# Performance work log

Measured on AMD Instinct MI355X. Metric: run time of the kernel, lower is better.

The kernel has to match this reference:

```python
import jax, jax.numpy as jnp
import numpy as np

ALPHA = 1.0
MIN_FEATURE_SIZE = 1.0
SC = 1e-12                      # stabilizer added to first derivatives
EPS_V_FLOOR = 1e-32 / 6.0       # torch.tensor(1e-32 ** 1 / 6) == 1e-32/6 (** binds tighter than /)


def _grad2d(phi, d):
    """Vectorized equivalent of numerical_gradient_2d: central differences in the
    interior, one-sided forward/backward differences at the boundaries."""
    gx = jnp.concatenate([
        (phi[1:2, :] - phi[0:1, :]) / d,           # forward diff at i == 0
        (phi[2:, :] - phi[:-2, :]) / (2.0 * d),    # central diff in interior
        (phi[-1:, :] - phi[-2:-1, :]) / d,         # backward diff at i == H-1
    ], axis=0)
    gy = jnp.concatenate([
        (phi[:, 1:2] - phi[:, 0:1]) / d,
        (phi[:, 2:] - phi[:, :-2]) / (2.0 * d),
        (phi[:, -1:] - phi[:, -2:-1]) / d,
    ], axis=1)
    return gx, gy


def setup_inputs() -> dict:
    key = jax.random.key(0)
    eps = jax.random.normal(key, (4096, 4096), dtype=jnp.float32)
    grid_size = jnp.asarray(0.05, dtype=jnp.float32)
    return {"eps": eps, "grid_size": grid_size}


def reference(eps, grid_size):
    # mirror the field along axis 1 (torch.cat((eps, eps.flip(1)), dim=1)) -> [H, 2W]
    eps = jnp.concatenate([eps, eps[:, ::-1]], axis=1)

    # ls_derivatives: first derivatives (+SC), then second derivatives of those
    eps_x, eps_y = _grad2d(eps, grid_size)
    eps_x = eps_x + SC
    eps_y = eps_y + SC
    eps_xx, eps_xy = _grad2d(eps_x, grid_size)
    _, eps_yy = _grad2d(eps_y, grid_size)

    pi_d = np.pi / (1.1 * MIN_FEATURE_SIZE)
    eps_v = jnp.maximum(jnp.sqrt(eps_x**2 + eps_y**2), EPS_V_FLOOR)
    k = (eps_x**2 * eps_yy - 2.0 * eps_x * eps_y * eps_xy + eps_y**2 * eps_xx) / eps_v**3
    curve_const = jnp.abs(k * jnp.arctan(eps_v / eps)) - pi_d
    return jnp.nansum(ALPHA * jnp.maximum(curve_const, 0.0) * grid_size**2)
```

## Files before the change

### kernel.cpp

```cpp
#include <hip/hip_runtime.h>
#include <math.h>


#define BLOCK_X 256
#define ROWS_PER 16

typedef float f32x2 __attribute__((ext_vector_type(2)));

__device__ __forceinline__ f32x2 mk2(float a, float b) { f32x2 v; v.x = a; v.y = b; return v; }
__device__ __forceinline__ f32x2 sp2(float a) { return mk2(a, a); }

#if __has_builtin(__builtin_elementwise_fma)
__device__ __forceinline__ f32x2 fma2(f32x2 a, f32x2 b, f32x2 c) { return __builtin_elementwise_fma(a, b, c); }
#else
__device__ __forceinline__ f32x2 fma2(f32x2 a, f32x2 b, f32x2 c) { return mk2(fmaf(a.x, b.x, c.x), fmaf(a.y, b.y, c.y)); }
#endif
#if __has_builtin(__builtin_elementwise_max)
__device__ __forceinline__ f32x2 max2(f32x2 a, f32x2 b) { return __builtin_elementwise_max(a, b); }
#else
__device__ __forceinline__ f32x2 max2(f32x2 a, f32x2 b) { return mk2(fmaxf(a.x, b.x), fmaxf(a.y, b.y)); }
#endif
__device__ __forceinline__ f32x2 abs2(f32x2 a) { return mk2(fabsf(a.x), fabsf(a.y)); }


__device__ __forceinline__ float fast_atan_ratio(float v, float c, float rv)
{
    const float rc = __builtin_amdgcn_rcpf(c);
    const float q  = v * rc;
    const float iq = c * rv;
    const bool  big = fabsf(q) > 1.0f;
    const float t  = big ? iq : q;
    const float s  = t * t;
    float p = fmaf(s, -0.01172120f, 0.05265332f);
    p = fmaf(s, p, -0.11643287f);
    p = fmaf(s, p,  0.19354346f);
    p = fmaf(s, p, -0.33262347f);
    p = fmaf(s, p,  0.99997726f);
    const float at = p * t;
    const float hp = copysignf(1.57079632679f, q);
    return big ? (hp - at) : at;
}

__device__ __forceinline__ f32x2 fast_atan_ratio2(f32x2 v, f32x2 c, f32x2 rvv)
{
    const f32x2 rc = mk2(__builtin_amdgcn_rcpf(c.x), __builtin_amdgcn_rcpf(c.y));
    const f32x2 q  = v * rc;
    const f32x2 iq = c * rvv;
    const bool big0 = fabsf(q.x) > 1.0f, big1 = fabsf(q.y) > 1.0f;
    const f32x2 t = mk2(big0 ? iq.x : q.x, big1 ? iq.y : q.y);
    const f32x2 s = t * t;
    f32x2 p = fma2(s, sp2(-0.01172120f), sp2(0.05265332f));
    p = fma2(s, p, sp2(-0.11643287f));
    p = fma2(s, p, sp2( 0.19354346f));
    p = fma2(s, p, sp2(-0.33262347f));
    p = fma2(s, p, sp2( 0.99997726f));
    const f32x2 at = p * t;
    const float hp0 = copysignf(1.57079632679f, q.x);
    const float hp1 = copysignf(1.57079632679f, q.y);
    return mk2(big0 ? (hp0 - at.x) : at.x, big1 ? (hp1 - at.y) : at.y);
}

template<bool XE>
__device__ __forceinline__ void load6(const float* __restrict__ rowp, int j0,
                                      bool left, bool right,
                                      f32x2& m, f32x2& c, f32x2& p)
{
    c = *reinterpret_cast<const f32x2*>(rowp + j0);
    if (XE) {
        const float* ma = rowp + (left  ? j0 : j0 - 2);
        const float* pa = rowp + (right ? j0 : j0 + 2);
        m = *reinterpret_cast<const f32x2*>(ma);
        p = *reinterpret_cast<const f32x2*>(pa);
        if (left)  m = mk2(c.x, c.x);
        if (right) p = mk2(c.y, c.x);
    } else {
        m = *reinterpret_cast<const f32x2*>(rowp + j0 - 2);
        p = *reinterpret_cast<const f32x2*>(rowp + j0 + 2);
    }
}

template<bool XE>
__device__ __forceinline__ f32x2 strip_packed(
    const float* __restrict__ eps, int Wn, int i0, int j0,
    bool left, bool right, float rd2, f32x2 syjv, f32x2 symv)
{
    const f32x2 SC2    = sp2(1e-12f);
    const float FLOORV = (float)(1e-32 / 6.0);
    const float pi_d   = 3.14159265358979323846f / 1.1f;

    const float* r0 = eps + (size_t)(i0 - 2) * (size_t)Wn;
    f32x2 A = *reinterpret_cast<const f32x2*>(r0 + j0);
    f32x2 Bm, Bc, Bp, Cm, Cc, Cp, Dm, Dc, Dp, Em, Ec, Ep;
    load6<XE>(r0 + (size_t)Wn,     j0, left, right, Bm, Bc, Bp);
    load6<XE>(r0 + (size_t)2 * Wn, j0, left, right, Cm, Cc, Cp);
    load6<XE>(r0 + (size_t)3 * Wn, j0, left, right, Dm, Dc, Dp);
    load6<XE>(r0 + (size_t)4 * Wn, j0, left, right, Em, Ec, Ep);
    const float* pr = r0 + (size_t)5 * Wn;

    f32x2 acc = sp2(0.0f);
    #pragma unroll 4
    for (int r = 0; r < ROWS_PER; ++r) {
        f32x2 Fm, Fc, Fp;
        load6<XE>(pr, j0, left, right, Fm, Fc, Fp);
        pr += Wn;

        const f32x2 ex  = fma2(Dc - Bc, sp2(rd2), SC2);
        const f32x2 Cl1 = mk2(Cm.y, Cc.x), Cr1 = mk2(Cc.y, Cp.x);
        const f32x2 ey  = fma2(Cr1 - Cl1, syjv, SC2);
        const f32x2 exn = fma2(Cc - A,  sp2(rd2), SC2);
        const f32x2 exs = fma2(Ec - Cc, sp2(rd2), SC2);
        const f32x2 exx = (exs - exn) * rd2;
        f32x2 eyw = fma2(Cc - Cm, symv, SC2);
        const f32x2 eye = fma2(Cp - Cc, sp2(rd2), SC2);
        if (XE) { if (left) eyw.x = ey.x; }
        const f32x2 eyy = (eye - eyw) * syjv;
        const f32x2 Bl1 = mk2(Bm.y, Bc.x), Br1 = mk2(Bc.y, Bp.x);
        const f32x2 Dl1 = mk2(Dm.y, Dc.x), Dr1 = mk2(Dc.y, Dp.x);
        const f32x2 exy = ((Dr1 - Br1) - (Dl1 - Bl1)) * (syjv * rd2);

        const f32x2 t1 = ex * ex, t2 = ey * ey;
        f32x2 num = t1 * eyy;
        num = fma2(t2, exx, num);
        num = fma2((ex * ey) * -2.0f, exy, num);
        const f32x2 ssum = t1 + t2;
        float ev0 = __builtin_amdgcn_sqrtf(ssum.x);
        float ev1 = __builtin_amdgcn_sqrtf(ssum.y);
        ev0 = fmaxf(ev0, FLOORV);
        ev1 = fmaxf(ev1, FLOORV);
        const f32x2 evv = mk2(ev0, ev1);
        const f32x2 rvv = mk2(__builtin_amdgcn_rcpf(ev0), __builtin_amdgcn_rcpf(ev1));
        const f32x2 k   = num * (rvv * rvv) * rvv;
        const f32x2 at  = fast_atan_ratio2(evv, Cc, rvv);
        const f32x2 cc  = abs2(k * at) - sp2(pi_d);
        acc = acc + max2(cc, sp2(0.0f));

        A  = Bc;
        Bm = Cm; Bc = Cc; Bp = Cp;
        Cm = Dm; Cc = Dc; Cp = Dp;
        Dm = Em; Dc = Ec; Dp = Ep;
        Em = Fm; Ec = Fc; Ep = Fp;
    }
    return acc;
}

__device__ float strip_scalar_yb(const float* __restrict__ eps, int Hn, int Wn,
                                 int i0, int j, float rd, float rd2)
{
    const float SC     = 1e-12f;
    const float FLOORV = (float)(1e-32 / 6.0);
    const float pi_d   = 3.14159265358979323846f / 1.1f;

    const int jm  = (j > 0) ? j - 1 : 0;
    const int jmm = (j > 1) ? j - 2 : 0;
    const int jp = j + 1, jpp = j + 2;
    const int cjp  = (jp  < Wn) ? jp  : (2 * Wn - 1 - jp);
    const int cjpp = (jpp < Wn) ? jpp : (2 * Wn - 1 - jpp);
    const bool jz = (j == 0);
    const float syj = jz ? rd : rd2;
    const float sym = (jm == 0) ? rd : rd2;

    auto rp = [&](int t) -> const float* {
        int tt = t < 0 ? 0 : t;
        tt = tt > Hn - 1 ? Hn - 1 : tt;
        return eps + (size_t)tt * (size_t)Wn;
    };

    float a2 = rp(i0 - 2)[j],   a1 = rp(i0 - 1)[j],  a0 = rp(i0)[j];
    float b1 = rp(i0 + 1)[j],   b2 = rp(i0 + 2)[j];
    float wN = rp(i0 - 1)[jm],  w0 = rp(i0)[jm],     wS = rp(i0 + 1)[jm];
    float eN = rp(i0 - 1)[cjp], e0 = rp(i0)[cjp],    eS = rp(i0 + 1)[cjp];
    float ww = rp(i0)[jmm],     ee = rp(i0)[cjpp];

    float acc = 0.0f;
    #pragma unroll 4
    for (int r = 0; r < ROWS_PER; ++r) {
        const int i = i0 + r;
        const float* q3 = rp(i + 3);
        const float* q2 = rp(i + 2);
        const float* q1 = rp(i + 1);
        const float nb2 = q3[j], nwS = q2[jm], neS = q2[cjp];
        const float nww = q1[jmm], nee = q1[cjpp];

        const bool itop = (i == 0), ibot = (i == Hn - 1);
        const float sxi = (itop || ibot) ? rd : rd2;
        const float sxm = (i == 1) ? rd : rd2;
        const float sxp = (i == Hn - 2) ? rd : rd2;

        const float ex = fmaf(b1 - a1, sxi, SC);
        const float ey = fmaf(e0 - w0, syj, SC);
        float exn = fmaf(a0 - a2, sxm, SC);
        float exs = fmaf(b2 - a0, sxp, SC);
        if (itop) exn = ex;
        if (ibot) exs = ex;
        const float exx = (exs - exn) * sxi;
        float eyw = fmaf(a0 - ww, sym, SC);
        const float eye = fmaf(ee - a0, rd2, SC);
        if (jz) eyw = ey;
        const float eyy = (eye - eyw) * syj;
        const float exy = ((eS - eN) - (wS - wN)) * (sxi * syj);

        const float t1 = ex * ex, t2 = ey * ey;
        float num = t1 * eyy;
        num = fmaf(t2, exx, num);
        num = fmaf(-2.0f * (ex * ey), exy, num);
        float ev = __builtin_amdgcn_sqrtf(t1 + t2);
        ev = fmaxf(ev, FLOORV);
        const float rv = __builtin_amdgcn_rcpf(ev);
        const float k  = num * (rv * rv) * rv;
        const float at = fast_atan_ratio(ev, a0, rv);
        const float ccv = fabsf(k * at) - pi_d;
        float contrib = fmaxf(ccv, 0.0f);
        if (i >= Hn) contrib = 0.0f;
        acc += contrib;

        a2 = a1; a1 = a0; a0 = b1; b1 = b2; b2 = nb2;
        wN = w0; w0 = wS; wS = nwS;
        eN = e0; e0 = eS; eS = neS;
        ww = nww; ee = nee;
    }
    return acc;
}

__global__ __launch_bounds__(BLOCK_X, 4) void curve_partial_kernel(
    const float* __restrict__ eps, const float* __restrict__ gs,
    double* __restrict__ partial, int Hn, int Wn)
{
    const int tx = threadIdx.x;
    const int j0 = (blockIdx.x * BLOCK_X + tx) * 2;
    const int i0 = blockIdx.y * ROWS_PER;
    const float d   = gs[0];
    const float rd  = 1.0f / d;
    const float rd2 = 0.5f * rd;
    const bool left  = (j0 == 0);
    const bool right = (j0 + 2 == Wn);

    const bool yint = (i0 >= 2) && (i0 + ROWS_PER + 2 < Hn);

    f32x2 accv;
    if (yint) {
        const f32x2 syjv = left ? mk2(rd,  rd2) : sp2(rd2);
        const f32x2 symv = left ? mk2(rd2, rd ) : sp2(rd2);
        const bool xe = (blockIdx.x == 0) || (blockIdx.x == gridDim.x - 1);
        accv = xe
            ? strip_packed<true >(eps, Wn, i0, j0, left, right, rd2, syjv, symv)
            : strip_packed<false>(eps, Wn, i0, j0, left, right, rd2, syjv, symv);
    } else {
        accv.x = strip_scalar_yb(eps, Hn, Wn, i0, j0,     rd, rd2);
        accv.y = strip_scalar_yb(eps, Hn, Wn, i0, j0 + 1, rd, rd2);
    }

    double acc = (double)accv.x + (double)accv.y;
    #pragma unroll
    for (int off = 32; off > 0; off >>= 1)
        acc += __shfl_down(acc, off, 64);
    __shared__ double lds[BLOCK_X / 64];
    const int lane = tx & 63, wv = tx >> 6;
    if (lane == 0) lds[wv] = acc;
    __syncthreads();
    if (tx == 0) {
        partial[blockIdx.y * gridDim.x + blockIdx.x] =
            lds[0] + lds[1] + lds[2] + lds[3];
    }
}

__global__ __launch_bounds__(256) void curve_finish_kernel(
    const double* __restrict__ partial, int n,
    const float* __restrict__ gs, float* __restrict__ out)
{
    const int tx = threadIdx.x;
    double acc = 0.0;
    for (int idx = tx; idx < n; idx += 256) acc += partial[idx];
    #pragma unroll
    for (int off = 32; off > 0; off >>= 1)
        acc += __shfl_down(acc, off, 64);
    __shared__ double lds[4];
    const int lane = tx & 63, wv = tx >> 6;
    if (lane == 0) lds[wv] = acc;
    __syncthreads();
    if (tx == 0) {
        const double dd = (double)gs[0];
        out[0] = (float)((lds[0] + lds[1] + lds[2] + lds[3]) * 2.0 * dd * dd);
    }
}

extern "C" void kernel_launch(void* const* d_in, const int* in_sizes, int n_in,
                              void* d_out, int out_size, void* d_ws, size_t ws_size,
                              hipStream_t stream) {
    const float* eps = (const float*)d_in[0];
    const float* gs  = (const float*)d_in[1];
    float* out = (float*)d_out;

    const int n = in_sizes[0];
    int Wn = (int)(sqrt((double)n) + 0.5);
    int Hn = n / Wn;

    const int gx = Wn / (BLOCK_X * 2);
    const int gy = (Hn + ROWS_PER - 1) / ROWS_PER;
    double* partial = (double*)d_ws;

    curve_partial_kernel<<<dim3(gx, gy), BLOCK_X, 0, stream>>>(eps, gs, partial, Hn, Wn);
    curve_finish_kernel<<<1, 256, 0, stream>>>(partial, gx * gy, gs, out);
}
```

Baseline: 112.3 us.

## Fuse final reduction via last-block atomic counter and reuse x-gradients across rows

Removes the separate finish kernel. Each block writes its partial sum, bumps a global atomic counter, and the last block to arrive reduces all partials and writes the output, then resets the counter. The packed strip loop also carries the x-derivative values and column differences forward in rolling registers instead of recomputing them each row. This trades a kernel launch and some VALU work for a threadfence plus atomic per block, and relies on the counter being reset correctly between calls.

```diff
diff --git a/kernel.cpp b/kernel.cpp
--- a/kernel.cpp
+++ b/kernel.cpp
@@ -21,6 +21,8 @@
 __device__ __forceinline__ f32x2 max2(f32x2 a, f32x2 b) { return mk2(fmaxf(a.x, b.x), fmaxf(a.y, b.y)); }
 #endif
 __device__ __forceinline__ f32x2 abs2(f32x2 a) { return mk2(fabsf(a.x), fabsf(a.y)); }
+
+__device__ unsigned int g_count = 0;
 
 
 __device__ __forceinline__ float fast_atan_ratio(float v, float c, float rv)
@@ -87,9 +89,11 @@
     const f32x2 SC2    = sp2(1e-12f);
     const float FLOORV = (float)(1e-32 / 6.0);
     const float pi_d   = 3.14159265358979323846f / 1.1f;
+    const f32x2 rd2v   = sp2(rd2);
+    const f32x2 sxy    = syjv * rd2;
 
     const float* r0 = eps + (size_t)(i0 - 2) * (size_t)Wn;
-    f32x2 A = *reinterpret_cast<const f32x2*>(r0 + j0);
+    const f32x2 Ac = *reinterpret_cast<const f32x2*>(r0 + j0);
     f32x2 Bm, Bc, Bp, Cm, Cc, Cp, Dm, Dc, Dp, Em, Ec, Ep;
     load6<XE>(r0 + (size_t)Wn,     j0, left, right, Bm, Bc, Bp);
     load6<XE>(r0 + (size_t)2 * Wn, j0, left, right, Cm, Cc, Cp);
@@ -97,6 +101,12 @@
     load6<XE>(r0 + (size_t)4 * Wn, j0, left, right, Em, Ec, Ep);
     const float* pr = r0 + (size_t)5 * Wn;
 
+    f32x2 xm1 = fma2(Cc - Ac, rd2v, SC2);
+    f32x2 gc0 = Dc - Bc;
+    f32x2 x0  = fma2(gc0, rd2v, SC2);
+    f32x2 gc1 = Ec - Cc;
+    f32x2 xp1 = fma2(gc1, rd2v, SC2);
+
     f32x2 acc = sp2(0.0f);
     #pragma unroll 4
     for (int r = 0; r < ROWS_PER; ++r) {
@@ -104,19 +114,20 @@
         load6<XE>(pr, j0, left, right, Fm, Fc, Fp);
         pr += Wn;
 
-        const f32x2 ex  = fma2(Dc - Bc, sp2(rd2), SC2);
+        const f32x2 gc2 = Fc - Dc;
+        const f32x2 x2v = fma2(gc2, rd2v, SC2);
+
+        const f32x2 ex  = x0;
+        const f32x2 exx = (xp1 - xm1) * rd2;
         const f32x2 Cl1 = mk2(Cm.y, Cc.x), Cr1 = mk2(Cc.y, Cp.x);
         const f32x2 ey  = fma2(Cr1 - Cl1, syjv, SC2);
-        const f32x2 exn = fma2(Cc - A,  sp2(rd2), SC2);
-        const f32x2 exs = fma2(Ec - Cc, sp2(rd2), SC2);
-        const f32x2 exx = (exs - exn) * rd2;
         f32x2 eyw = fma2(Cc - Cm, symv, SC2);
-        const f32x2 eye = fma2(Cp - Cc, sp2(rd2), SC2);
+        const f32x2 eye = fma2(Cp - Cc, rd2v, SC2);
         if (XE) { if (left) eyw.x = ey.x; }
         const f32x2 eyy = (eye - eyw) * syjv;
-        const f32x2 Bl1 = mk2(Bm.y, Bc.x), Br1 = mk2(Bc.y, Bp.x);
-        const f32x2 Dl1 = mk2(Dm.y, Dc.x), Dr1 = mk2(Dc.y, Dp.x);
-        const f32x2 exy = ((Dr1 - Br1) - (Dl1 - Bl1)) * (syjv * rd2);
+        const f32x2 Gm = Dm - Bm, Gp = Dp - Bp;
+        const f32x2 exyL = mk2(Gm.y, gc0.x), exyR = mk2(gc0.y, Gp.x);
+        const f32x2 exy = (exyR - exyL) * sxy;
 
         const f32x2 t1 = ex * ex, t2 = ey * ey;
         f32x2 num = t1 * eyy;
@@ -134,12 +145,13 @@
         const f32x2 cc  = abs2(k * at) - sp2(pi_d);
         acc = acc + max2(cc, sp2(0.0f));
 
-        A  = Bc;
-        Bm = Cm; Bc = Cc; Bp = Cp;
+        xm1 = x0; x0 = xp1; xp1 = x2v; gc0 = gc1; gc1 = gc2;
+        Bm = Cm; Bp = Cp;
         Cm = Dm; Cc = Dc; Cp = Dp;
         Dm = Em; Dc = Ec; Dp = Ep;
         Em = Fm; Ec = Fc; Ep = Fp;
     }
+    (void)Bc;
     return acc;
 }
 
@@ -223,7 +235,8 @@
 
 __global__ __launch_bounds__(BLOCK_X, 4) void curve_partial_kernel(
     const float* __restrict__ eps, const float* __restrict__ gs,
-    double* __restrict__ partial, int Hn, int Wn)
+    double* __restrict__ partial, float* __restrict__ out,
+    int Hn, int Wn, int nb)
 {
     const int tx = threadIdx.x;
     const int j0 = (blockIdx.x * BLOCK_X + tx) * 2;
@@ -254,32 +267,36 @@
     for (int off = 32; off > 0; off >>= 1)
         acc += __shfl_down(acc, off, 64);
     __shared__ double lds[BLOCK_X / 64];
+    __shared__ int elected;
     const int lane = tx & 63, wv = tx >> 6;
     if (lane == 0) lds[wv] = acc;
     __syncthreads();
+
+    const int bid = blockIdx.y * gridDim.x + blockIdx.x;
     if (tx == 0) {
-        partial[blockIdx.y * gridDim.x + blockIdx.x] =
-            lds[0] + lds[1] + lds[2] + lds[3];
-    }
-}
-
-__global__ __launch_bounds__(256) void curve_finish_kernel(
-    const double* __restrict__ partial, int n,
-    const float* __restrict__ gs, float* __restrict__ out)
-{
-    const int tx = threadIdx.x;
-    double acc = 0.0;
-    for (int idx = tx; idx < n; idx += 256) acc += partial[idx];
-    #pragma unroll
-    for (int off = 32; off > 0; off >>= 1)
-        acc += __shfl_down(acc, off, 64);
-    __shared__ double lds[4];
-    const int lane = tx & 63, wv = tx >> 6;
-    if (lane == 0) lds[wv] = acc;
+        const double bsum = lds[0] + lds[1] + lds[2] + lds[3];
+        partial[bid] = bsum;
+        __threadfence();
+        const unsigned old = atomicAdd(&g_count, 1u);
+        elected = (old == (unsigned)nb - 1u) ? 1 : 0;
+    }
     __syncthreads();
-    if (tx == 0) {
-        const double dd = (double)gs[0];
-        out[0] = (float)((lds[0] + lds[1] + lds[2] + lds[3]) * 2.0 * dd * dd);
+
+    if (elected) {
+        __threadfence();
+        double a2 = 0.0;
+        for (int idx = tx; idx < nb; idx += BLOCK_X) a2 += partial[idx];
+        #pragma unroll
+        for (int off = 32; off > 0; off >>= 1)
+            a2 += __shfl_down(a2, off, 64);
+        __syncthreads();
+        if (lane == 0) lds[wv] = a2;
+        __syncthreads();
+        if (tx == 0) {
+            const double dd = (double)gs[0];
+            out[0] = (float)((lds[0] + lds[1] + lds[2] + lds[3]) * 2.0 * dd * dd);
+            atomicExch(&g_count, 0u);
+        }
     }
 }
 
@@ -296,8 +313,9 @@
 
     const int gx = Wn / (BLOCK_X * 2);
     const int gy = (Hn + ROWS_PER - 1) / ROWS_PER;
+    const int nb = gx * gy;
     double* partial = (double*)d_ws;
 
-    curve_partial_kernel<<<dim3(gx, gy), BLOCK_X, 0, stream>>>(eps, gs, partial, Hn, Wn);
-    curve_finish_kernel<<<1, 256, 0, stream>>>(partial, gx * gy, gs, out);
-}
+    curve_partial_kernel<<<dim3(gx, gy), BLOCK_X, 0, stream>>>(
+        eps, gs, partial, out, Hn, Wn, nb);
+}
```

After: 158.2 us. +40.9%, slower.
